# Kernel optimization log

Hardware: AMD Instinct MI355X
Metric: run time of the kernel (lower is better)

## Reference

```python
import jax, jax.numpy as jnp
import numpy as np

N_EMBD = 768
N_HEAD = 12
HEAD_SIZE = N_EMBD // N_HEAD
LN_EPS = 1e-5


def setup_inputs() -> dict:
    key = jax.random.key(0)
    ks = jax.random.split(key, 12)
    s = 0.02
    B, T, C = 8, 1024, N_EMBD
    return {
        "x":  jax.random.normal(ks[0], (B, T, C), dtype=jnp.float32),
        # per-head q/k/v projections packed as [C, H*hs] (concat of head outputs)
        "Wq": jax.random.normal(ks[1], (C, C), dtype=jnp.float32) * s,
        "Wk": jax.random.normal(ks[2], (C, C), dtype=jnp.float32) * s,
        "Wv": jax.random.normal(ks[3], (C, C), dtype=jnp.float32) * s,
        "Wo": jax.random.normal(ks[4], (C, C), dtype=jnp.float32) * s,
        "bo": jnp.zeros((C,), dtype=jnp.float32),
        "W1": jax.random.normal(ks[5], (C, 4 * C), dtype=jnp.float32) * s,
        "b1": jnp.zeros((4 * C,), dtype=jnp.float32),
        "W2": jax.random.normal(ks[6], (4 * C, C), dtype=jnp.float32) * s,
        "b2": jnp.zeros((C,), dtype=jnp.float32),
        "g1": jnp.ones((C,), dtype=jnp.float32),
        "be1": jnp.zeros((C,), dtype=jnp.float32),
        "g2": jnp.ones((C,), dtype=jnp.float32),
        "be2": jnp.zeros((C,), dtype=jnp.float32),
    }


def _layernorm(x, g, b):
    mu = jnp.mean(x, axis=-1, keepdims=True)
    var = jnp.mean(jnp.square(x - mu), axis=-1, keepdims=True)
    return (x - mu) * jax.lax.rsqrt(var + LN_EPS) * g + b


def _block(x, Wq, Wk, Wv, Wo, bo, W1, b1, W2, b2, g1, be1, g2, be2):
    B, T, C = x.shape
    H, hs = N_HEAD, HEAD_SIZE
    h = _layernorm(x, g1, be1)
    q = (h @ Wq).reshape(B, T, H, hs)
    k = (h @ Wk).reshape(B, T, H, hs)
    v = (h @ Wv).reshape(B, T, H, hs)
    # NOTE: original code scales by n_embd**-0.5 (C from x.shape), not head_size**-0.5
    scores = jnp.einsum("bthd,bshd->bhts", q, k) * (C ** -0.5)
    causal = jnp.tril(jnp.ones((T, T), dtype=bool))  # [T,T]
    scores = jnp.where(causal, scores, -jnp.inf)
    attn = jax.nn.softmax(scores, axis=-1)  # [B,H,T,T]
    o = jnp.einsum("bhts,bshd->bthd", attn, v).reshape(B, T, C)
    x = x + o @ Wo + bo
    h2 = _layernorm(x, g2, be2)
    ff = jax.nn.gelu(h2 @ W1 + b1, approximate=False) @ W2 + b2
    return x + ff


def reference(x, Wq, Wk, Wv, Wo, bo, W1, b1, W2, b2, g1, be1, g2, be2):
    return _block(x, Wq, Wk, Wv, Wo, bo, W1, b1, W2, b2, g1, be1, g2, be2)
```

## Files before the change

### kernel.cpp

```cpp
#include <hip/hip_runtime.h>
#include <math.h>
#include <stdint.h>

typedef unsigned short u16;
typedef unsigned int u32;
typedef __attribute__((ext_vector_type(8))) __bf16 bf16x8;
typedef __attribute__((ext_vector_type(4))) float f32x4;

#define AS1 __attribute__((address_space(1)))
#define AS3 __attribute__((address_space(3)))

__device__ __forceinline__ void stage16(const void* g, void* l) {
    __builtin_amdgcn_global_load_lds((const AS1 void*)(uintptr_t)g,
                                     (AS3 void*)(uintptr_t)l, 16, 0, 0);
}

__device__ __forceinline__ u16 f2bf(float f) {
    u32 u = __float_as_uint(f);
    u += 0x7fffu + ((u >> 16) & 1u);
    return (u16)(u >> 16);
}

__global__ __launch_bounds__(256) void ln_kernel(const float* __restrict__ x,
                                                 const float* __restrict__ g,
                                                 const float* __restrict__ b,
                                                 u16* __restrict__ out) {
    __shared__ float s8[8];
    int row = blockIdx.x;
    int tid = threadIdx.x;
    const int w = tid >> 6;
    const float* xr = x + (size_t)row * 768;
    float x0 = xr[tid], x1 = xr[tid + 256], x2 = xr[tid + 512];

    float sum = x0 + x1 + x2;
#pragma unroll
    for (int off = 32; off; off >>= 1) sum += __shfl_xor(sum, off);
    if ((tid & 63) == 0) s8[w] = sum;
    __syncthreads();
    float mu = (s8[0] + s8[1] + s8[2] + s8[3]) * (1.0f / 768.0f);

    float d0 = x0 - mu, d1 = x1 - mu, d2 = x2 - mu;
    float sq = d0 * d0 + d1 * d1 + d2 * d2;
#pragma unroll
    for (int off = 32; off; off >>= 1) sq += __shfl_xor(sq, off);
    if ((tid & 63) == 0) s8[4 + w] = sq;
    __syncthreads();
    float var = (s8[4] + s8[5] + s8[6] + s8[7]) * (1.0f / 768.0f);
    float rs = rsqrtf(var + 1e-5f);

    u16* orow = out + (size_t)row * 768;
    orow[tid]       = f2bf(d0 * rs * g[tid]       + b[tid]);
    orow[tid + 256] = f2bf(d1 * rs * g[tid + 256] + b[tid + 256]);
    orow[tid + 512] = f2bf(d2 * rs * g[tid + 512] + b[tid + 512]);
}

__global__ __launch_bounds__(256) void transpose_bf16(const float* __restrict__ W,
                                                      u16* __restrict__ Wt,
                                                      int K, int N) {
    __shared__ float t[32][33];
    int tx = threadIdx.x, ty = threadIdx.y;
    int n0 = blockIdx.x * 32, k0 = blockIdx.y * 32;
#pragma unroll
    for (int j = 0; j < 32; j += 8)
        t[ty + j][tx] = W[(size_t)(k0 + ty + j) * N + n0 + tx];
    __syncthreads();
#pragma unroll
    for (int j = 0; j < 32; j += 8)
        Wt[(size_t)(n0 + ty + j) * K + k0 + tx] = f2bf(t[tx][ty + j]);
}

__global__ __launch_bounds__(256) void transpose4_768(const float* __restrict__ Wq,
                                                      const float* __restrict__ Wk,
                                                      const float* __restrict__ Wv,
                                                      const float* __restrict__ Wo,
                                                      u16* __restrict__ Wqkvt,
                                                      u16* __restrict__ Wot) {
    __shared__ float t[32][33];
    const int z = blockIdx.z;
    const float* W = (z == 0) ? Wq : (z == 1) ? Wk : (z == 2) ? Wv : Wo;
    u16* Wt = (z == 3) ? Wot : (Wqkvt + (size_t)z * 768 * 768);
    int tx = threadIdx.x, ty = threadIdx.y;
    int n0 = blockIdx.x * 32, k0 = blockIdx.y * 32;
#pragma unroll
    for (int j = 0; j < 32; j += 8)
        t[ty + j][tx] = W[(size_t)(k0 + ty + j) * 768 + n0 + tx];
    __syncthreads();
#pragma unroll
    for (int j = 0; j < 32; j += 8)
        Wt[(size_t)(n0 + ty + j) * 768 + k0 + tx] = f2bf(t[tx][ty + j]);
}

__global__ __launch_bounds__(256) void vt_kernel(const u16* __restrict__ qkv,
                                                 u16* __restrict__ Vt) {
    __shared__ u16 t[32][34];
    const int tx = threadIdx.x, ty = threadIdx.y;
    const int s0 = blockIdx.x * 32, d0 = blockIdx.y * 32, bh = blockIdx.z;
    const int b = bh / 12, h = bh % 12;
#pragma unroll
    for (int j = 0; j < 32; j += 8)
        t[ty + j][tx] = qkv[((size_t)(b * 1024) + s0 + ty + j) * 2304 + 1536 + h * 64 + d0 + tx];
    __syncthreads();
#pragma unroll
    for (int j = 0; j < 32; j += 8)
        Vt[((size_t)bh * 64 + d0 + ty + j) * 1024 + s0 + tx] = t[tx][ty + j];
}

__global__ __launch_bounds__(256, 3) void gemm_k32(
    const u16* __restrict__ A, const u16* __restrict__ Bt,
    const float* __restrict__ bias, const float* __restrict__ res,
    float* __restrict__ outF, u16* __restrict__ outB,
    int N, int K, int act) {
    __shared__ char lds[49152];
    const int tid = threadIdx.x, lane = tid & 63, wid = tid >> 6;
    const int l15 = lane & 15, lk = lane >> 4;
    const int wrow = (wid >> 1) * 64, wcol = (wid & 1) * 64;

    int wg = blockIdx.y * gridDim.x + blockIdx.x;
    const int nwg = gridDim.x * gridDim.y;
    wg = (wg & 7) * (nwg >> 3) + (wg >> 3);
    const int brow = (wg / gridDim.x) * 128;
    const int bcol = (wg % gridDim.x) * 128;

    const size_t K2 = (size_t)K * 2;
    const char* Abase = (const char*)A + (size_t)brow * K2;
    const char* Bbase = (const char*)Bt + (size_t)bcol * K2;

    int srow[2], scol[2];
#pragma unroll
    for (int j = 0; j < 2; ++j) {
        const int L = j * 4096 + tid * 16;
        srow[j] = L >> 6;
        scol[j] = (L & 63) ^ (((srow[j] >> 1) & 3) << 4);
    }

    const int nt = K >> 5;

    auto stage_tile = [&](int t, char* dst) {
#pragma unroll
        for (int j = 0; j < 2; ++j) {
            const size_t off = (size_t)srow[j] * K2 + (size_t)t * 64 + scol[j];
            stage16(Abase + off, dst + j * 4096 + tid * 16);
            stage16(Bbase + off, dst + 8192 + j * 4096 + tid * 16);
        }
    };

    f32x4 acc[4][4] = {};

    stage_tile(0, lds);
    stage_tile(1, lds + 16384);

    auto iter = [&](int t, char* buf, char* nxt) {
        if (t + 1 < nt) asm volatile("s_waitcnt vmcnt(4)\n\ts_barrier" ::: "memory");
        else            asm volatile("s_waitcnt vmcnt(0)\n\ts_barrier" ::: "memory");
        __builtin_amdgcn_sched_barrier(0);

        if (t + 2 < nt) stage_tile(t + 2, nxt);

        const char* As = buf;
        const char* Bs = buf + 8192;
        bf16x8 af[4], bfv[4];
#pragma unroll
        for (int m = 0; m < 4; ++m) {
            const int row = wrow + m * 16 + l15;
            af[m] = *(const bf16x8*)(As + row * 64 +
                                     ((lk * 16) ^ (((row >> 1) & 3) << 4)));
        }
#pragma unroll
        for (int n = 0; n < 4; ++n) {
            const int row = wcol + n * 16 + l15;
            bfv[n] = *(const bf16x8*)(Bs + row * 64 +
                                      ((lk * 16) ^ (((row >> 1) & 3) << 4)));
        }
        __builtin_amdgcn_s_setprio(1);
#pragma unroll
        for (int m = 0; m < 4; ++m)
#pragma unroll
            for (int n = 0; n < 4; ++n)
                acc[m][n] = __builtin_amdgcn_mfma_f32_16x16x32_bf16(af[m], bfv[n], acc[m][n], 0, 0, 0);
        __builtin_amdgcn_s_setprio(0);
    };

    for (int t = 0; t < nt; t += 3) {
        iter(t,     lds,         lds + 32768);
        iter(t + 1, lds + 16384, lds);
        iter(t + 2, lds + 32768, lds + 16384);
    }

#pragma unroll
    for (int m = 0; m < 4; ++m)
#pragma unroll
        for (int n = 0; n < 4; ++n)
#pragma unroll
            for (int r = 0; r < 4; ++r) {
                int row = brow + wrow + m * 16 + lk * 4 + r;
                int col = bcol + wcol + n * 16 + l15;
                float v = acc[m][n][r];
                if (bias) v += bias[col];
                if (act) v = 0.5f * v * (1.0f + erff(v * 0.70710678118654752f));
                if (res) v += res[(size_t)row * N + col];
                if (outB) outB[(size_t)row * N + col] = f2bf(v);
                else outF[(size_t)row * N + col] = v;
            }
}

__global__ __launch_bounds__(256) void attn_mfma(const u16* __restrict__ qkv,
                                                 const u16* __restrict__ Vt,
                                                 u16* __restrict__ obf) {
    __shared__ char lds[40960];
    const int tid = threadIdx.x, lane = tid & 63, w = tid >> 6;
    const int g = lane >> 4, l15 = lane & 15;

    int wg = blockIdx.y * gridDim.x + blockIdx.x;
    const int nwg = gridDim.x * gridDim.y;
    wg = (wg & 7) * (nwg >> 3) + (wg >> 3);
    const int qb = 15 - (wg & 15);
    const int bh = wg >> 4;
    const int h = bh % 12, b = bh / 12;
    const int t0 = qb * 64;
    const float scale = 0.03608439182435161f;

    const size_t qrow = ((size_t)b * 1024 + t0 + 16 * w + l15) * 2304 + h * 64;
    const bf16x8 qf0 = *(const bf16x8*)(qkv + qrow + 8 * g);
    const bf16x8 qf1 = *(const bf16x8*)(qkv + qrow + 8 * g + 32);

    const int sub = ((lane & 7) * 16) ^ ((lane >> 3) << 4);
    const int r0 = 16 * w + (lane >> 3);
    const char* kSrc = (const char*)qkv + ((size_t)(b * 1024 + r0) * 2304 + 768 + h * 64) * 2 + sub;
    const char* vSrc = (const char*)Vt + ((size_t)(bh * 64 + r0) * 1024) * 2 + sub;
    const int dstOff = 2 * w * 1024 + lane * 16;

    stage16(kSrc,            lds + dstOff);
    stage16(kSrc + 8 * 4608, lds + dstOff + 1024);
    stage16(vSrc,            lds + 8192 + dstOff);
    stage16(vSrc + 8 * 2048, lds + 8192 + dstOff + 1024);
    kSrc += 64 * 4608; vSrc += 128;
    __syncthreads();

    const int swzA = (l15 & 7) << 4;
    float m_r[4] = {-1e30f, -1e30f, -1e30f, -1e30f};
    float l_r[4] = {0.f, 0.f, 0.f, 0.f};
    f32x4 oacc[4] = {};
    char* Pw = lds + 32768 + w * 2048;

    for (int c = 0; c <= qb; ++c) {
        if (c < qb) {
            char* dst = lds + ((c + 1) & 1) * 16384;
            stage16(kSrc,            dst + dstOff);
            stage16(kSrc + 8 * 4608, dst + dstOff + 1024);
            stage16(vSrc,            dst + 8192 + dstOff);
            stage16(vSrc + 8 * 2048, dst + 8192 + dstOff + 1024);
            kSrc += 64 * 4608; vSrc += 128;
            asm volatile("s_waitcnt vmcnt(4)\n\ts_barrier" ::: "memory");
        } else {
            asm volatile("s_waitcnt vmcnt(0)\n\ts_barrier" ::: "memory");
        }
        __builtin_amdgcn_sched_barrier(0);

        const char* bufK = lds + (c & 1) * 16384;
        const char* bufV = bufK + 8192;

        f32x4 sacc[4] = {};
#pragma unroll
        for (int st = 0; st < 4; ++st) {
            const char* krow = bufK + (l15 + 16 * st) * 128;
            const bf16x8 kf0 = *(const bf16x8*)(krow + ((16 * g) ^ swzA));
            const bf16x8 kf1 = *(const bf16x8*)(krow + ((16 * g + 64) ^ swzA));
            sacc[st] = __builtin_amdgcn_mfma_f32_16x16x32_bf16(qf0, kf0, sacc[st], 0, 0, 0);
            sacc[st] = __builtin_amdgcn_mfma_f32_16x16x32_bf16(qf1, kf1, sacc[st], 0, 0, 0);
        }

        const bool diag = (c == qb);
#pragma unroll
        for (int r = 0; r < 4; ++r) {
            float sv0 = sacc[0][r] * scale, sv1 = sacc[1][r] * scale;
            float sv2 = sacc[2][r] * scale, sv3 = sacc[3][r] * scale;
            if (diag) {
                const int trel = 16 * w + 4 * g + r;
                if (l15 +  0 > trel) sv0 = -1e30f;
                if (l15 + 16 > trel) sv1 = -1e30f;
                if (l15 + 32 > trel) sv2 = -1e30f;
                if (l15 + 48 > trel) sv3 = -1e30f;
            }
            float mx = fmaxf(fmaxf(sv0, sv1), fmaxf(sv2, sv3));
#pragma unroll
            for (int off = 1; off < 16; off <<= 1) mx = fmaxf(mx, __shfl_xor(mx, off));
            if (mx > m_r[r]) {
                const float corr = __expf(m_r[r] - mx);
                m_r[r] = mx;
                l_r[r] *= corr;
                oacc[0][r] *= corr; oacc[1][r] *= corr;
                oacc[2][r] *= corr; oacc[3][r] *= corr;
            }
            const float p0 = __expf(sv0 - m_r[r]), p1 = __expf(sv1 - m_r[r]);
            const float p2 = __expf(sv2 - m_r[r]), p3 = __expf(sv3 - m_r[r]);
            float ps = p0 + p1 + p2 + p3;
#pragma unroll
            for (int off = 1; off < 16; off <<= 1) ps += __shfl_xor(ps, off);
            l_r[r] += ps;
            const int q = 4 * g + r;
            char* pr = Pw + q * 128;
            const int sw = (q & 7) << 4;
            *(u16*)(pr + ((l15 * 2 +  0) ^ sw)) = f2bf(p0);
            *(u16*)(pr + ((l15 * 2 + 32) ^ sw)) = f2bf(p1);
            *(u16*)(pr + ((l15 * 2 + 64) ^ sw)) = f2bf(p2);
            *(u16*)(pr + ((l15 * 2 + 96) ^ sw)) = f2bf(p3);
        }

#pragma unroll
        for (int kc = 0; kc < 2; ++kc) {
            const bf16x8 pa = *(const bf16x8*)(Pw + l15 * 128 + ((16 * g + 64 * kc) ^ swzA));
#pragma unroll
            for (int dt = 0; dt < 4; ++dt) {
                const int d = l15 + 16 * dt;
                const bf16x8 vf = *(const bf16x8*)(bufV + d * 128 +
                                   ((16 * g + 64 * kc) ^ ((d & 7) << 4)));
                oacc[dt] = __builtin_amdgcn_mfma_f32_16x16x32_bf16(pa, vf, oacc[dt], 0, 0, 0);
            }
        }
        asm volatile("s_barrier" ::: "memory");
    }

    const size_t orow0 = ((size_t)b * 1024 + t0 + 16 * w) * 768 + h * 64;
#pragma unroll
    for (int r = 0; r < 4; ++r) {
        const float inv = 1.0f / l_r[r];
        const size_t orow = orow0 + (size_t)(4 * g + r) * 768;
#pragma unroll
        for (int dt = 0; dt < 4; ++dt)
            obf[orow + 16 * dt + l15] = f2bf(oacc[dt][r] * inv);
    }
}

extern "C" void kernel_launch(void* const* d_in, const int* in_sizes, int n_in,
                              void* d_out, int out_size, void* d_ws, size_t ws_size,
                              hipStream_t stream) {
    const float* x   = (const float*)d_in[0];
    const float* Wq  = (const float*)d_in[1];
    const float* Wk  = (const float*)d_in[2];
    const float* Wv  = (const float*)d_in[3];
    const float* Wo  = (const float*)d_in[4];
    const float* bo  = (const float*)d_in[5];
    const float* W1  = (const float*)d_in[6];
    const float* b1  = (const float*)d_in[7];
    const float* W2  = (const float*)d_in[8];
    const float* b2  = (const float*)d_in[9];
    const float* g1  = (const float*)d_in[10];
    const float* be1 = (const float*)d_in[11];
    const float* g2  = (const float*)d_in[12];
    const float* be2 = (const float*)d_in[13];
    float* out = (float*)d_out;

    char* ws = (char*)d_ws;
    u16* qkv_bf = (u16*)(ws);
    u16* ff1_bf = (u16*)(ws);
    float* x2   = (float*)(ws + 50331648);
    u16* h_bf   = (u16*)(ws + 75497472);
    u16* o_bf   = (u16*)(ws + 88080384);
    u16* Wqkvt  = (u16*)(ws + 100663296);
    u16* W1t    = (u16*)(ws + 104202240);
    u16* W2t    = (u16*)(ws + 108920832);
    u16* Wot    = (u16*)(ws + 113639424);
    u16* Vt     = (u16*)(ws + 114819072);

    dim3 tb(32, 8);
    transpose4_768<<<dim3(24, 24, 4), tb, 0, stream>>>(Wq, Wk, Wv, Wo, Wqkvt, Wot);
    transpose_bf16<<<dim3(96, 24), tb, 0, stream>>>(W1, W1t, 768, 3072);
    transpose_bf16<<<dim3(24, 96), tb, 0, stream>>>(W2, W2t, 3072, 768);

    ln_kernel<<<8192, 256, 0, stream>>>(x, g1, be1, h_bf);
    gemm_k32<<<dim3(18, 64), 256, 0, stream>>>(h_bf, Wqkvt, nullptr, nullptr, nullptr, qkv_bf, 2304, 768, 0);
    vt_kernel<<<dim3(32, 2, 96), tb, 0, stream>>>(qkv_bf, Vt);
    attn_mfma<<<dim3(16, 96), 256, 0, stream>>>(qkv_bf, Vt, o_bf);
    gemm_k32<<<dim3(6, 64), 256, 0, stream>>>(o_bf, Wot, bo, x, x2, nullptr, 768, 768, 0);
    ln_kernel<<<8192, 256, 0, stream>>>(x2, g2, be2, h_bf);
    gemm_k32<<<dim3(24, 64), 256, 0, stream>>>(h_bf, W1t, b1, nullptr, nullptr, ff1_bf, 3072, 768, 1);
    gemm_k32<<<dim3(6, 64), 256, 0, stream>>>(ff1_bf, W2t, b2, x2, out, nullptr, 768, 3072, 0);
}
```

Baseline: 370.2 us.

## Add 256x256-tile 512-thread GEMM kernel for QKV and FC1 projections

Adds a new bf16 MFMA GEMM with 256x256 output tiles, 8 waves each computing a 128x64 sub-tile, double-buffered LDS staging via global_load_lds, and a swizzled LDS layout. It replaces the 128x128 kernel for the QKV and first FFN projections, where N is large. The aim is more data reuse per loaded tile and more MFMA work per barrier. In exchange the grids get smaller (288 and 384 workgroups), which may leave CUs underused, and each thread holds more accumulators, which raises register pressure.

```diff
diff --git a/kernel.cpp b/kernel.cpp
--- a/kernel.cpp
+++ b/kernel.cpp
@@ -103,6 +103,97 @@
 #pragma unroll
     for (int j = 0; j < 32; j += 8)
         Vt[((size_t)bh * 64 + d0 + ty + j) * 1024 + s0 + tx] = t[tx][ty + j];
+}
+
+__global__ __launch_bounds__(512, 2) void gemm256(
+    const u16* __restrict__ A, const u16* __restrict__ Bt,
+    const float* __restrict__ bias,
+    u16* __restrict__ outB, int N, int K, int act) {
+    __shared__ char lds[65536];
+    const int tid = threadIdx.x, lane = tid & 63, wid = tid >> 6;
+    const int l15 = lane & 15, lk = lane >> 4;
+    const int wr = wid >> 2, wc = wid & 3;
+
+    int wg = blockIdx.y * gridDim.x + blockIdx.x;
+    const int nwg = gridDim.x * gridDim.y;
+    wg = (wg & 7) * (nwg >> 3) + (wg >> 3);
+    const int brow = (wg / gridDim.x) * 256;
+    const int bcol = (wg % gridDim.x) * 256;
+
+    const size_t K2 = (size_t)K * 2;
+    const char* Abase = (const char*)A + (size_t)brow * K2;
+    const char* Bbase = (const char*)Bt + (size_t)bcol * K2;
+
+    int srow[2], scol[2];
+#pragma unroll
+    for (int j = 0; j < 2; ++j) {
+        const int L = j * 8192 + tid * 16;
+        srow[j] = L >> 6;
+        scol[j] = (L & 63) ^ (((srow[j] >> 1) & 3) << 4);
+    }
+
+    const int nt = K >> 5;
+
+    auto stage_tile = [&](int t, char* dst) {
+#pragma unroll
+        for (int j = 0; j < 2; ++j) {
+            const size_t off = (size_t)srow[j] * K2 + (size_t)t * 64 + scol[j];
+            stage16(Abase + off, dst + j * 8192 + tid * 16);
+            stage16(Bbase + off, dst + 16384 + j * 8192 + tid * 16);
+        }
+    };
+
+    f32x4 acc[8][4] = {};
+
+    stage_tile(0, lds);
+
+    for (int t = 0; t < nt; ++t) {
+        if (t + 1 < nt) {
+            stage_tile(t + 1, lds + ((t + 1) & 1) * 32768);
+            asm volatile("s_waitcnt vmcnt(4)\n\ts_barrier" ::: "memory");
+        } else {
+            asm volatile("s_waitcnt vmcnt(0)\n\ts_barrier" ::: "memory");
+        }
+        __builtin_amdgcn_sched_barrier(0);
+
+        const char* As = lds + (t & 1) * 32768;
+        const char* Bs = As + 16384;
+        bf16x8 af[8], bfv[4];
+#pragma unroll
+        for (int m = 0; m < 8; ++m) {
+            const int row = wr * 128 + m * 16 + l15;
+            af[m] = *(const bf16x8*)(As + row * 64 +
+                                     ((lk * 16) ^ (((row >> 1) & 3) << 4)));
+        }
+#pragma unroll
+        for (int n = 0; n < 4; ++n) {
+            const int row = wc * 64 + n * 16 + l15;
+            bfv[n] = *(const bf16x8*)(Bs + row * 64 +
+                                      ((lk * 16) ^ (((row >> 1) & 3) << 4)));
+        }
+        __builtin_amdgcn_s_setprio(1);
+#pragma unroll
+        for (int m = 0; m < 8; ++m)
+#pragma unroll
+            for (int n = 0; n < 4; ++n)
+                acc[m][n] = __builtin_amdgcn_mfma_f32_16x16x32_bf16(af[m], bfv[n], acc[m][n], 0, 0, 0);
+        __builtin_amdgcn_s_setprio(0);
+        __builtin_amdgcn_s_barrier();
+    }
+
+#pragma unroll
+    for (int m = 0; m < 8; ++m)
+#pragma unroll
+        for (int n = 0; n < 4; ++n)
+#pragma unroll
+            for (int r = 0; r < 4; ++r) {
+                int row = brow + wr * 128 + m * 16 + lk * 4 + r;
+                int col = bcol + wc * 64 + n * 16 + l15;
+                float v = acc[m][n][r];
+                if (bias) v += bias[col];
+                if (act) v = 0.5f * v * (1.0f + erff(v * 0.70710678118654752f));
+                outB[(size_t)row * N + col] = f2bf(v);
+            }
 }
 
 __global__ __launch_bounds__(256, 3) void gemm_k32(
@@ -368,11 +459,11 @@
     transpose_bf16<<<dim3(24, 96), tb, 0, stream>>>(W2, W2t, 3072, 768);
 
     ln_kernel<<<8192, 256, 0, stream>>>(x, g1, be1, h_bf);
-    gemm_k32<<<dim3(18, 64), 256, 0, stream>>>(h_bf, Wqkvt, nullptr, nullptr, nullptr, qkv_bf, 2304, 768, 0);
+    gemm256<<<dim3(9, 32), 512, 0, stream>>>(h_bf, Wqkvt, nullptr, qkv_bf, 2304, 768, 0);
     vt_kernel<<<dim3(32, 2, 96), tb, 0, stream>>>(qkv_bf, Vt);
     attn_mfma<<<dim3(16, 96), 256, 0, stream>>>(qkv_bf, Vt, o_bf);
     gemm_k32<<<dim3(6, 64), 256, 0, stream>>>(o_bf, Wot, bo, x, x2, nullptr, 768, 768, 0);
     ln_kernel<<<8192, 256, 0, stream>>>(x2, g2, be2, h_bf);
-    gemm_k32<<<dim3(24, 64), 256, 0, stream>>>(h_bf, W1t, b1, nullptr, nullptr, ff1_bf, 3072, 768, 1);
+    gemm256<<<dim3(12, 32), 512, 0, stream>>>(h_bf, W1t, b1, ff1_bf, 3072, 768, 1);
     gemm_k32<<<dim3(6, 64), 256, 0, stream>>>(ff1_bf, W2t, b2, x2, out, nullptr, 768, 3072, 0);
 }
```

Measured after the change: 411.7 us. 1.11x slower.
